# Performance work log

Measured on AMD Instinct MI355X. Metric: run time of the kernel, lower is better.

The kernel has to match this reference:

```python
import jax, jax.numpy as jnp
import numpy as np

B, C, LH, LW = 2, 64, 64, 64
KSIZE = 3
HO, WO = LH * 4, LW * 4          # fold output size
HR, WR = HO - KSIZE + 1, WO - KSIZE + 1  # ref spatial size so unfold L == fold L


def setup_inputs() -> dict:
    key = jax.random.key(0)
    k1, k2, k3 = jax.random.split(key, 3)
    lr = jax.random.normal(k1, (B, C, LH, LW), dtype=jnp.float32)
    ref = jax.random.normal(k2, (B, C, HR, WR), dtype=jnp.float32)
    L = HR * WR
    index_map = jax.random.randint(k3, (B, L), 0, L)
    return {"lr": lr, "ref": ref, "index_map": index_map}


def reference(lr, ref, index_map):
    b, c, lh, lw = lr.shape
    k = KSIZE
    ho, wo = lh * 4, lw * 4
    hr, wr = ref.shape[2], ref.shape[3]
    # 'same' padding for ksize=3, stride=1, rate=1 -> reflect pad 1 on each side
    padded = jnp.pad(ref, ((0, 0), (0, 0), (1, 1), (1, 1)), mode='reflect')
    # im2col / unfold, torch channel ordering (C, kh, kw): [B, C, k, k, hr, wr]
    patches = jnp.stack(
        [jnp.stack([padded[:, :, i:i + hr, j:j + wr] for j in range(k)], axis=2)
         for i in range(k)], axis=2)
    patches = patches.reshape(b, c * k * k, hr * wr)  # [B, C*k*k, L]
    # indexed gather along the patch (L) dimension
    idx = jnp.broadcast_to(index_map[:, None, :], patches.shape)
    warped = jnp.take_along_axis(patches, idx, axis=2)
    # col2im / fold with overlap-add to (ho, wo), kernel k, stride 1, pad 0
    hb, wb = ho - k + 1, wo - k + 1  # == hr, wr
    p = warped.reshape(b, c, k, k, hb, wb)
    out = jnp.zeros((b, c, ho, wo), dtype=ref.dtype)
    for i in range(k):
        for j in range(k):
            out = out.at[:, :, i:i + hb, j:j + wb].add(p[:, :, i, j])
    return out
```

## Files before the change

### kernel.cpp

```cpp
#include <hip/hip_runtime.h>
#include <hip/hip_fp16.h>


#define B_   2
#define C_   64
#define HR_  254
#define WR_  254
#define HO_  256
#define WO_  256
#define L_   (HR_ * WR_)
#define PPLANE_ ((size_t)HO_ * WO_ * 16)

__global__ __launch_bounds__(256) void pad_transpose_b16(
    const float* __restrict__ ref, _Float16* __restrict__ P)
{
    __shared__ unsigned short srow[C_][66];

    unsigned bid  = blockIdx.x;
    unsigned b    = bid >> 10;
    unsigned rest = bid & 1023u;
    unsigned py   = rest >> 2;
    unsigned x0   = (rest & 3u) * 64u;
    int ry = (py == 0) ? 1 : ((py == HO_ - 1) ? HR_ - 2 : (int)py - 1);

    const float* rrow = ref + ((size_t)b * C_) * (HR_ * WR_) + (size_t)ry * WR_;
    unsigned tid = threadIdx.x;

    #pragma unroll
    for (unsigned k = 0; k < 16; ++k) {
        unsigned e = k * 256u + tid;
        unsigned c = e >> 6, u = e & 63u;
        unsigned px = x0 + u;
        int rx = (px == 0) ? 1 : ((px == WO_ - 1) ? WR_ - 2 : (int)px - 1);
        float v = __builtin_nontemporal_load(&rrow[(size_t)c * (HR_ * WR_) + rx]);
        _Float16 h = (_Float16)v;
        srow[c][u] = __builtin_bit_cast(unsigned short, h);
    }
    __syncthreads();

    #pragma unroll
    for (unsigned it = 0; it < 8; ++it) {
        unsigned w   = it * 256u + tid;
        unsigned g4  = w >> 9;
        unsigned rem = w & 511u;
        unsigned pxl = rem >> 3;
        unsigned cp  = rem & 7u;
        unsigned c0  = g4 * 16u + cp * 2u;
        unsigned pk  = (unsigned)srow[c0][pxl]
                     | ((unsigned)srow[c0 + 1][pxl] << 16);
        _Float16* pg = P + ((size_t)(b * 4u + g4) * PPLANE_
                            + ((size_t)py * WO_ + x0 + pxl) * 16u + cp * 2u);
        *reinterpret_cast<unsigned*>(pg) = pk;
    }
}

__global__ __launch_bounds__(256) void warp_gather5_kernel(
    const _Float16* __restrict__ P,
    const int*      __restrict__ index_map,
    float*          __restrict__ out)
{
    __shared__ unsigned sbase[3][132];

    unsigned bid   = blockIdx.x;
    unsigned combo = bid & 7u;
    unsigned inner = bid >> 3;
    unsigned b     = combo >> 2;
    unsigned g4    = combo & 3u;
    unsigned y     = inner >> 1;
    unsigned x0    = (inner & 1u) * 128u;
    unsigned tid   = threadIdx.x;

    const int* imb = index_map + (size_t)b * L_;
    for (unsigned e = tid; e < 3 * 130; e += 256) {
        unsigned r    = e / 130;
        unsigned ccol = e - r * 130;
        int ly = (int)y - 2 + (int)r;
        int lx = (int)(x0 + ccol) - 2;
        unsigned v = 0xFFFFFFFFu;
        if (ly >= 0 && ly < HR_ && lx >= 0 && lx < WR_) {
            unsigned src = (unsigned)imb[ly * WR_ + lx];
            unsigned sy  = src / WR_;
            unsigned sx  = src - sy * WR_;
            v = (sy * (unsigned)WO_ + sx) * 16u;
        }
        sbase[r][ccol] = v;
    }
    __syncthreads();

    unsigned wv   = tid >> 6;
    unsigned lane = tid & 63u;
    unsigned pq   = lane >> 1;
    unsigned h    = lane & 1u;
    unsigned pxl  = wv * 32u + pq;
    const _Float16* Pp = P + (size_t)combo * PPLANE_;

    uint4 raw[9];
    float msk[9];
    #pragma unroll
    for (int k = 0; k < 9; ++k) {
        int i = k / 3, j = k % 3;
        unsigned v = sbase[2 - i][pxl + 2u - (unsigned)j];
        bool valid = (v != 0xFFFFFFFFu);
        unsigned off = (valid ? v : 0u)
                     + (unsigned)((i * WO_ + j) * 16) + h * 8u;
        msk[k] = valid ? 1.0f : 0.0f;
        raw[k] = *reinterpret_cast<const uint4*>(Pp + off);
    }

    float acc[8] = {0.f, 0.f, 0.f, 0.f, 0.f, 0.f, 0.f, 0.f};
    #pragma unroll
    for (int k = 0; k < 9; ++k) {
        union { uint4 u; _Float16 hh[8]; } cv;
        cv.u = raw[k];
        #pragma unroll
        for (int m = 0; m < 8; ++m) {
            acc[m] = fmaf((float)cv.hh[m], msk[k], acc[m]);
        }
    }

    float* ob = out + ((size_t)b * C_) * (HO_ * WO_) + (size_t)y * WO_ + x0;
    #pragma unroll
    for (int m = 0; m < 8; ++m) {
        unsigned ch = g4 * 16u + h * 8u + (unsigned)m;
        __builtin_nontemporal_store(acc[m],
            ob + (size_t)ch * (HO_ * WO_) + pxl);
    }
}

extern "C" void kernel_launch(void* const* d_in, const int* in_sizes, int n_in,
                              void* d_out, int out_size, void* d_ws, size_t ws_size,
                              hipStream_t stream) {
    const float* ref       = (const float*)d_in[1];
    const int*   index_map = (const int*)d_in[2];
    float*       out       = (float*)d_out;

    _Float16* P = (_Float16*)d_ws;
    pad_transpose_b16<<<dim3(B_ * HO_ * 4), dim3(256), 0, stream>>>(ref, P);
    warp_gather5_kernel<<<dim3(B_ * HO_ * 8), dim3(256), 0, stream>>>(P, index_map, out);
}
```

Before: 41.54 us.

## Widen channel-interleaved fp16 planes from 16 to 32 channels per pixel

The padded half-precision ref buffer is reorganised into two planes of 32 interleaved channels per pixel instead of four planes of 16. Each gather now reads 64 contiguous bytes per source pixel, and each block covers 64 output pixels times 32 channels with fewer index_map lookups per channel. Blocks are also remapped so that y-halves, batch and channel-half are spread across the grid. The aim is fewer, wider random gathers and less redundant index decoding, at the cost of narrower 64-pixel output row segments per block.

Result: faster. 40.62 us (-2.2%).

```diff
diff --git a/kernel.cpp b/kernel.cpp
--- a/kernel.cpp
+++ b/kernel.cpp
@@ -9,9 +9,9 @@
 #define HO_  256
 #define WO_  256
 #define L_   (HR_ * WR_)
-#define PPLANE_ ((size_t)HO_ * WO_ * 16)
+#define PPLANE32_ ((size_t)HO_ * WO_ * 32)
 
-__global__ __launch_bounds__(256) void pad_transpose_b16(
+__global__ __launch_bounds__(256) void pad_transpose_b32(
     const float* __restrict__ ref, _Float16* __restrict__ P)
 {
     __shared__ unsigned short srow[C_][66];
@@ -40,40 +40,41 @@
 
     #pragma unroll
     for (unsigned it = 0; it < 8; ++it) {
-        unsigned w   = it * 256u + tid;
-        unsigned g4  = w >> 9;
-        unsigned rem = w & 511u;
-        unsigned pxl = rem >> 3;
-        unsigned cp  = rem & 7u;
-        unsigned c0  = g4 * 16u + cp * 2u;
-        unsigned pk  = (unsigned)srow[c0][pxl]
-                     | ((unsigned)srow[c0 + 1][pxl] << 16);
-        _Float16* pg = P + ((size_t)(b * 4u + g4) * PPLANE_
-                            + ((size_t)py * WO_ + x0 + pxl) * 16u + cp * 2u);
+        unsigned w    = it * 256u + tid;
+        unsigned half = w >> 10;
+        unsigned rem  = w & 1023u;
+        unsigned pxl  = rem >> 4;
+        unsigned cp   = rem & 15u;
+        unsigned c0   = half * 32u + cp * 2u;
+        unsigned pk   = (unsigned)srow[c0][pxl]
+                      | ((unsigned)srow[c0 + 1][pxl] << 16);
+        _Float16* pg = P + ((size_t)(b * 2u + half) * PPLANE32_
+                            + ((size_t)py * WO_ + x0 + pxl) * 32u + cp * 2u);
         *reinterpret_cast<unsigned*>(pg) = pk;
     }
 }
 
-__global__ __launch_bounds__(256) void warp_gather5_kernel(
+__global__ __launch_bounds__(256) void warp_gather6_kernel(
     const _Float16* __restrict__ P,
     const int*      __restrict__ index_map,
     float*          __restrict__ out)
 {
-    __shared__ unsigned sbase[3][132];
+    __shared__ unsigned sbase[3][66];
 
     unsigned bid   = blockIdx.x;
-    unsigned combo = bid & 7u;
+    unsigned slot  = bid & 7u;
     unsigned inner = bid >> 3;
-    unsigned b     = combo >> 2;
-    unsigned g4    = combo & 3u;
-    unsigned y     = inner >> 1;
-    unsigned x0    = (inner & 1u) * 128u;
+    unsigned b     = (slot >> 1) & 1u;
+    unsigned half  = slot & 1u;
+    unsigned yr    = slot >> 2;
+    unsigned y     = yr * 128u + (inner >> 2);
+    unsigned x0    = (inner & 3u) * 64u;
     unsigned tid   = threadIdx.x;
 
     const int* imb = index_map + (size_t)b * L_;
-    for (unsigned e = tid; e < 3 * 130; e += 256) {
-        unsigned r    = e / 130;
-        unsigned ccol = e - r * 130;
+    if (tid < 3 * 66) {
+        unsigned r    = tid / 66;
+        unsigned ccol = tid - r * 66;
         int ly = (int)y - 2 + (int)r;
         int lx = (int)(x0 + ccol) - 2;
         unsigned v = 0xFFFFFFFFu;
@@ -81,7 +82,7 @@
             unsigned src = (unsigned)imb[ly * WR_ + lx];
             unsigned sy  = src / WR_;
             unsigned sx  = src - sy * WR_;
-            v = (sy * (unsigned)WO_ + sx) * 16u;
+            v = (sy * (unsigned)WO_ + sx) * 32u;
         }
         sbase[r][ccol] = v;
     }
@@ -89,10 +90,10 @@
 
     unsigned wv   = tid >> 6;
     unsigned lane = tid & 63u;
-    unsigned pq   = lane >> 1;
-    unsigned h    = lane & 1u;
-    unsigned pxl  = wv * 32u + pq;
-    const _Float16* Pp = P + (size_t)combo * PPLANE_;
+    unsigned pq   = lane & 15u;
+    unsigned cg   = lane >> 4;
+    unsigned pxl  = wv * 16u + pq;
+    const _Float16* Pp = P + (size_t)(b * 2u + half) * PPLANE32_;
 
     uint4 raw[9];
     float msk[9];
@@ -102,7 +103,7 @@
         unsigned v = sbase[2 - i][pxl + 2u - (unsigned)j];
         bool valid = (v != 0xFFFFFFFFu);
         unsigned off = (valid ? v : 0u)
-                     + (unsigned)((i * WO_ + j) * 16) + h * 8u;
+                     + (unsigned)((i * WO_ + j) * 32) + cg * 8u;
         msk[k] = valid ? 1.0f : 0.0f;
         raw[k] = *reinterpret_cast<const uint4*>(Pp + off);
     }
@@ -121,7 +122,7 @@
     float* ob = out + ((size_t)b * C_) * (HO_ * WO_) + (size_t)y * WO_ + x0;
     #pragma unroll
     for (int m = 0; m < 8; ++m) {
-        unsigned ch = g4 * 16u + h * 8u + (unsigned)m;
+        unsigned ch = half * 32u + cg * 8u + (unsigned)m;
         __builtin_nontemporal_store(acc[m],
             ob + (size_t)ch * (HO_ * WO_) + pxl);
     }
@@ -135,6 +136,6 @@
     float*       out       = (float*)d_out;
 
     _Float16* P = (_Float16*)d_ws;
-    pad_transpose_b16<<<dim3(B_ * HO_ * 4), dim3(256), 0, stream>>>(ref, P);
-    warp_gather5_kernel<<<dim3(B_ * HO_ * 8), dim3(256), 0, stream>>>(P, index_map, out);
+    pad_transpose_b32<<<dim3(B_ * HO_ * 4), dim3(256), 0, stream>>>(ref, P);
+    warp_gather6_kernel<<<dim3(B_ * HO_ * 8), dim3(256), 0, stream>>>(P, index_map, out);
 }
```
